# Kernel tuning notes

Measured on AMD Instinct MI355X. Metric: run time of the kernel, lower is better.

Reference implementation:

```python
import jax, jax.numpy as jnp
import numpy as np

H = 256          # hidden_dim
K = 5            # num_mixtures
Z = 32           # latent_dim
A = 3            # action dim
B, T = 128, 512
IN = Z + A       # LSTM input features
MDN = K * (1 + 2 * Z)  # 325


def setup_inputs() -> dict:
    key = jax.random.key(0)
    ks = jax.random.split(key, 8)
    s_in = 1.0 / np.sqrt(IN)
    s_h = 1.0 / np.sqrt(H)
    return {
        "z_t": jax.random.normal(ks[0], (B, T, Z), jnp.float32),
        "a_t": jax.random.normal(ks[1], (B, T, A), jnp.float32),
        # LSTM params: fused gate kernels, gate order [i, f, g, o]
        "Wx": jax.random.normal(ks[2], (IN, 4 * H), jnp.float32) * s_in,
        "Wh": jax.random.normal(ks[3], (H, 4 * H), jnp.float32) * s_h,
        "b": jnp.zeros((4 * H,), jnp.float32),
        # MDN head Dense(325)
        "Wd": jax.random.normal(ks[4], (H, MDN), jnp.float32) * s_h,
        "bd": jnp.zeros((MDN,), jnp.float32),
    }


def _mdnrnn(z_t, a_t, Wx, Wh, b, Wd, bd):
    x = jnp.concatenate([z_t, a_t], axis=-1)          # (B,T,IN)
    # hoist the input projection out of the recurrence (same math)
    xproj = jnp.einsum("bti,ig->btg", x, Wx)          # (B,T,4H)
    xproj_t = jnp.swapaxes(xproj, 0, 1)               # (T,B,4H)
    bsz = x.shape[0]
    c0 = jnp.zeros((bsz, H), x.dtype)
    h0 = jnp.zeros((bsz, H), x.dtype)

    def step(carry, xp):
        c, h = carry
        gates = xp + h @ Wh + b                        # (B,4H)
        i, f, g, o = jnp.split(gates, 4, axis=-1)
        i = jax.nn.sigmoid(i)
        f = jax.nn.sigmoid(f)
        g = jnp.tanh(g)
        o = jax.nn.sigmoid(o)
        c = f * c + i * g
        h = o * jnp.tanh(c)
        return (c, h), h

    final_carry, hs = jax.lax.scan(step, (c0, h0), xproj_t)
    outputs = jnp.swapaxes(hs, 0, 1)                  # (B,T,H)

    mdn = outputs @ Wd + bd                           # (B,T,325)
    log_pi, mu, log_sigma = jnp.split(mdn, [K, K + K * Z * 2 // 2 + K * Z - K], axis=-1)
    # splits: [K, (1+Z)*K] -> log_pi (K), mu (K*Z), log_sigma (K*Z)
    log_pi, mu, log_sigma = mdn[..., :K], mdn[..., K:K + K * Z], mdn[..., K + K * Z:]
    bt = outputs.shape[:2]
    mu = mu.reshape(bt[0], bt[1], K, Z)
    log_sigma = log_sigma.reshape(bt[0], bt[1], K, Z)
    log_pi = jax.nn.log_softmax(log_pi, axis=-1)
    sigma = jnp.exp(log_sigma) + 1e-06
    return log_pi, mu, sigma, final_carry


def reference(z_t, a_t, Wx, Wh, b, Wd, bd):
    return _mdnrnn(z_t, a_t, Wx, Wh, b, Wd, bd)
```

## Files before the change

kernel.cpp:

```cpp
#include <hip/hip_runtime.h>
#include <hip/hip_bf16.h>
#include <math.h>

#define T_LEN 512
#define B_SZ  128
#define H_DIM 256
#define G_DIM 1024
#define IN_D  35
#define MDN_D 325
#define K_MIX 5

#define NSLICE 4
#define BG     2
#define NGRP   64

static constexpr long OFF_MU    = 327680L;
static constexpr long OFF_SIGMA = 10813440L;
static constexpr long OFF_C     = 21299200L;
static constexpr long OFF_H     = 21331968L;

static constexpr size_t WS_OUT = 0;
static constexpr size_t WS_HG  = 33554432;

typedef unsigned uint2v  __attribute__((ext_vector_type(2)));
typedef float    float2v __attribute__((ext_vector_type(2)));
typedef float    float4v __attribute__((ext_vector_type(4)));

__device__ __forceinline__ float fast_sigmoid(float x) { return 1.0f / (1.0f + __expf(-x)); }
__device__ __forceinline__ float fast_tanh(float x) {
    return 1.0f - 2.0f / (__expf(2.0f * x) + 1.0f);
}

__device__ __forceinline__ void pk_fma_lo(float2v& acc, float2v w, float2v h) {
    asm("v_pk_fma_f32 %0, %1, %2, %0 op_sel:[0,0,0] op_sel_hi:[1,0,1]"
        : "+v"(acc) : "v"(w), "v"(h));
}
__device__ __forceinline__ void pk_fma_hi(float2v& acc, float2v w, float2v h) {
    asm("v_pk_fma_f32 %0, %1, %2, %0 op_sel:[0,1,0] op_sel_hi:[1,1,1]"
        : "+v"(acc) : "v"(w), "v"(h));
}

__global__ __launch_bounds__(512, 1) void lstm6_kernel(
    const float* __restrict__ z_t, const float* __restrict__ a_t,
    const float* __restrict__ Wx,  const float* __restrict__ Wh,
    const float* __restrict__ bias,
    float* __restrict__ h_glb,
    __hip_bfloat16* __restrict__ outs,
    float* __restrict__ out_c, float* __restrict__ out_h)
{
    const int bid = blockIdx.x;
    const int gr  = bid & 63;
    const int s   = bid >> 6;
    const int tid = threadIdx.x;
    const int cg  = tid >> 2;
    const int kq  = tid & 3;
    const int lc0 = cg * 2;
    const int gate = lc0 >> 6;
    const int j0   = lc0 & 63;
    const int gcol0 = gate * 256 + s * 64 + j0;

    __shared__ __align__(16) float h_lds[BG][4][68];
    __shared__ __align__(16) float x_lds[BG][44];
    __shared__ __align__(16) float g_red[BG][256];

    for (int i = tid; i < BG * 4 * 68; i += 512) ((float*)h_lds)[i] = 0.0f;
    if (tid < BG * 9) { int b = tid / 9, k = tid - 9 * b; x_lds[b][35 + k] = 0.0f; }

    float2v W2[64];
    #pragma unroll
    for (int i = 0; i < 64; ++i) {
        const size_t r = (size_t)(kq * 64 + i) * G_DIM;
        W2[i].x = Wh[r + gcol0];
        W2[i].y = Wh[r + gcol0 + 1];
    }
    float2v X2[10];
    #pragma unroll
    for (int i = 0; i < 10; ++i) {
        int xk = kq * 10 + i;
        bool ok = (xk < IN_D);
        X2[i].x = ok ? Wx[(size_t)xk * G_DIM + gcol0]     : 0.0f;
        X2[i].y = ok ? Wx[(size_t)xk * G_DIM + gcol0 + 1] : 0.0f;
    }
    #pragma unroll
    for (int i = 0; i < 64; ++i) asm volatile("" : "+v"(W2[i]));
    #pragma unroll
    for (int i = 0; i < 10; ++i) asm volatile("" : "+v"(X2[i]));

    const int cb = tid >> 6;
    const int cj = tid & 63;
    const float bc0 = bias[0 * 256 + s * 64 + cj];
    const float bc1 = bias[1 * 256 + s * 64 + cj];
    const float bc2 = bias[2 * 256 + s * 64 + cj];
    const float bc3 = bias[3 * 256 + s * 64 + cj];
    float c_reg = 0.0f;

    const int q  = tid - 128;
    const int pb = (q >= 96) ? 1 : 0;
    const int pp = q - 96 * pb;
    const int pk0 = pp * 2;
    const int pkk = pk0 + ((pk0 >= s * 64) ? 64 : 0);

    const int batch0 = gr * BG;
    float* hg = h_glb + (size_t)gr * (2 * BG * H_DIM);

    if (tid >= 384 && tid < 448) {
        int qq = tid - 384, b = qq >> 5, k = qq & 31;
        x_lds[b][k] = z_t[((size_t)(batch0 + b) * T_LEN + 0) * 32 + k];
    } else if (tid >= 448 && tid < 448 + BG * 3) {
        int qq = tid - 448, b = (qq >= 3), k = qq - 3 * b;
        x_lds[b][32 + k] = a_t[((size_t)(batch0 + b) * T_LEN + 0) * 3 + k];
    }
    __syncthreads();

    for (int t = 0; t < T_LEN; ++t) {
        if (t > 0 && tid >= 128 && tid < 320) {
            const unsigned want = (unsigned)((t - 1) & 3);
            const float* ap = hg + ((t - 1) & 1) * (BG * H_DIM) + pb * H_DIM + pkk;
            uint2v u;
            do {
                asm volatile("global_load_dwordx2 %0, %1, off sc0 sc1\n\t"
                             "s_waitcnt vmcnt(0)"
                             : "=v"(u) : "v"(ap) : "memory");
            } while ((u.x & 3u) != want || (u.y & 3u) != want);
            float* dst = &h_lds[pb][pkk >> 6][pkk & 63];
            dst[0] = __uint_as_float(u.x);
            dst[1] = __uint_as_float(u.y);
        }
        __syncthreads();

        float2v acc0 = {0.0f, 0.0f}, acc1 = {0.0f, 0.0f};
        {
            const float4v* hp0 = (const float4v*)h_lds[0][kq];
            const float4v* hp1 = (const float4v*)h_lds[1][kq];
            #pragma unroll
            for (int i4 = 0; i4 < 16; ++i4) {
                float4v hv0 = hp0[i4];
                float4v hv1 = hp1[i4];
                float2v h0lo = __builtin_shufflevector(hv0, hv0, 0, 1);
                float2v h0hi = __builtin_shufflevector(hv0, hv0, 2, 3);
                float2v h1lo = __builtin_shufflevector(hv1, hv1, 0, 1);
                float2v h1hi = __builtin_shufflevector(hv1, hv1, 2, 3);
                pk_fma_lo(acc0, W2[4*i4+0], h0lo); pk_fma_lo(acc1, W2[4*i4+0], h1lo);
                pk_fma_hi(acc0, W2[4*i4+1], h0lo); pk_fma_hi(acc1, W2[4*i4+1], h1lo);
                pk_fma_lo(acc0, W2[4*i4+2], h0hi); pk_fma_lo(acc1, W2[4*i4+2], h1hi);
                pk_fma_hi(acc0, W2[4*i4+3], h0hi); pk_fma_hi(acc1, W2[4*i4+3], h1hi);
            }
            #pragma unroll
            for (int i = 0; i < 5; ++i) {
                float2v xv0 = *(const float2v*)&x_lds[0][kq * 10 + 2 * i];
                float2v xv1 = *(const float2v*)&x_lds[1][kq * 10 + 2 * i];
                pk_fma_lo(acc0, X2[2*i],   xv0); pk_fma_lo(acc1, X2[2*i],   xv1);
                pk_fma_hi(acc0, X2[2*i+1], xv0); pk_fma_hi(acc1, X2[2*i+1], xv1);
            }
        }
        float a00 = acc0.x, a01 = acc0.y, a10 = acc1.x, a11 = acc1.y;
        a00 += __shfl_xor(a00, 1, 64); a00 += __shfl_xor(a00, 2, 64);
        a01 += __shfl_xor(a01, 1, 64); a01 += __shfl_xor(a01, 2, 64);
        a10 += __shfl_xor(a10, 1, 64); a10 += __shfl_xor(a10, 2, 64);
        a11 += __shfl_xor(a11, 1, 64); a11 += __shfl_xor(a11, 2, 64);
        if (kq == 0) {
            g_red[0][lc0] = a00; g_red[0][lc0 + 1] = a01;
            g_red[1][lc0] = a10; g_red[1][lc0 + 1] = a11;
        }
        __syncthreads();

        if (tid < 128) {
            float gi = g_red[cb][      cj] + bc0;
            float gf = g_red[cb][ 64 + cj] + bc1;
            float gg = g_red[cb][128 + cj] + bc2;
            float go = g_red[cb][192 + cj] + bc3;
            float iv = fast_sigmoid(gi), fv = fast_sigmoid(gf), ov = fast_sigmoid(go);
            float gv = fast_tanh(gg);
            c_reg = fmaf(fv, c_reg, iv * gv);
            float hv = ov * fast_tanh(c_reg);
            unsigned u = (__float_as_uint(hv) & ~3u) | (unsigned)(t & 3);
            float* dst = hg + (t & 1) * (BG * H_DIM) + cb * H_DIM + s * 64 + cj;
            asm volatile("global_store_dword %0, %1, off sc0 sc1"
                         :: "v"(dst), "v"(u) : "memory");
            h_lds[cb][s][cj] = __uint_as_float(u);
            outs[((size_t)(batch0 + cb) * T_LEN + t) * H_DIM + s * 64 + cj] =
                __float2bfloat16(hv);
            if (t == T_LEN - 1) {
                out_c[(batch0 + cb) * H_DIM + s * 64 + cj] = c_reg;
                out_h[(batch0 + cb) * H_DIM + s * 64 + cj] = hv;
            }
        }
        if (t + 1 < T_LEN) {
            if (tid >= 384 && tid < 448) {
                int qq = tid - 384, b = qq >> 5, k = qq & 31;
                x_lds[b][k] = z_t[((size_t)(batch0 + b) * T_LEN + (t + 1)) * 32 + k];
            } else if (tid >= 448 && tid < 448 + BG * 3) {
                int qq = tid - 448, b = (qq >= 3), k = qq - 3 * b;
                x_lds[b][32 + k] = a_t[((size_t)(batch0 + b) * T_LEN + (t + 1)) * 3 + k];
            }
        }
    }
}

__global__ __launch_bounds__(256, 1) void mdn_kernel(
    const unsigned short* __restrict__ outputs, const float* __restrict__ Wd,
    const float* __restrict__ bd, float* __restrict__ out)
{
    __shared__ __align__(16) float hT[H_DIM * 16];
    __shared__ float lp[16][K_MIX];

    const int tid = threadIdx.x;
    const long row0 = (long)blockIdx.x * 16;

    for (int idx = tid; idx < H_DIM * 16; idx += 256) {
        int r = idx >> 8;
        int k = idx & (H_DIM - 1);
        unsigned int u = outputs[(row0 + r) * H_DIM + k];
        hT[k * 16 + r] = __uint_as_float(u << 16);
    }
    __syncthreads();

    const int  cA = tid;
    const int  cB = tid + 256;
    const bool vB = (cB < MDN_D);
    const float bA = bd[cA];
    const float bB = vB ? bd[cB] : 0.0f;
    float accA[16], accB[16];
    #pragma unroll
    for (int r = 0; r < 16; ++r) { accA[r] = bA; accB[r] = bB; }

    for (int k = 0; k < H_DIM; ++k) {
        float wA = Wd[(size_t)k * MDN_D + cA];
        float wB = vB ? Wd[(size_t)k * MDN_D + cB] : 0.0f;
        const float4* hp = (const float4*)(hT + k * 16);
        float4 h0 = hp[0], h1 = hp[1], h2 = hp[2], h3 = hp[3];
        float hr[16] = { h0.x,h0.y,h0.z,h0.w, h1.x,h1.y,h1.z,h1.w,
                         h2.x,h2.y,h2.z,h2.w, h3.x,h3.y,h3.z,h3.w };
        #pragma unroll
        for (int r = 0; r < 16; ++r) {
            accA[r] = fmaf(hr[r], wA, accA[r]);
            accB[r] = fmaf(hr[r], wB, accB[r]);
        }
    }

    float* out_mu = out + OFF_MU;
    float* out_sg = out + OFF_SIGMA;
    #pragma unroll
    for (int r = 0; r < 16; ++r) {
        long row = row0 + r;
        float v = accA[r];
        if (cA < K_MIX)            lp[r][cA] = v;
        else if (cA < K_MIX + 160) out_mu[row * 160 + (cA - K_MIX)] = v;
        else                       out_sg[row * 160 + (cA - 165)]   = __expf(v) + 1e-6f;
        if (vB)                    out_sg[row * 160 + (cB - 165)]   = __expf(accB[r]) + 1e-6f;
    }
    __syncthreads();

    if (tid < 16) {
        int r = tid;
        long row = row0 + r;
        float v0 = lp[r][0], v1 = lp[r][1], v2 = lp[r][2], v3 = lp[r][3], v4 = lp[r][4];
        float m = fmaxf(fmaxf(fmaxf(v0, v1), fmaxf(v2, v3)), v4);
        float sum = __expf(v0-m) + __expf(v1-m) + __expf(v2-m) + __expf(v3-m) + __expf(v4-m);
        float ls = m + __logf(sum);
        out[row*5 + 0] = v0 - ls;
        out[row*5 + 1] = v1 - ls;
        out[row*5 + 2] = v2 - ls;
        out[row*5 + 3] = v3 - ls;
        out[row*5 + 4] = v4 - ls;
    }
}

extern "C" void kernel_launch(void* const* d_in, const int* in_sizes, int n_in,
                              void* d_out, int out_size, void* d_ws, size_t ws_size,
                              hipStream_t stream)
{
    const float* z_t = (const float*)d_in[0];
    const float* a_t = (const float*)d_in[1];
    const float* Wx  = (const float*)d_in[2];
    const float* Wh  = (const float*)d_in[3];
    const float* b   = (const float*)d_in[4];
    const float* Wd  = (const float*)d_in[5];
    const float* bd  = (const float*)d_in[6];
    float* out = (float*)d_out;

    char* ws = (char*)d_ws;
    __hip_bfloat16* outs = (__hip_bfloat16*)(ws + WS_OUT);
    float* h_glb         = (float*)(ws + WS_HG);

    lstm6_kernel<<<NGRP * NSLICE, 512, 0, stream>>>(z_t, a_t, Wx, Wh, b,
                                                    h_glb, outs,
                                                    out + OFF_C, out + OFF_H);
    mdn_kernel<<<(B_SZ * T_LEN) / 16, 256, 0, stream>>>((const unsigned short*)outs,
                                                        Wd, bd, out);
}
```

Measured before the change: 1.192 ms.

## Pipeline spin-wait loads, double-buffer x input, widen MDN tile with packed FMA

The LSTM spin-wait on neighbouring slices' h values now keeps two global loads in flight instead of issuing one and waiting for it, which should cut polling latency on the serial recurrence. The per-step x input buffer in LDS is double-buffered so the prefetch of step t+1 cannot race with reads of step t. The MDN head kernel now handles 32 rows per block, uses a padded transposed LDS tile (stride 34), and accumulates with float2 vector FMAs that may map to packed FP32 math. This raises occupancy hints and reuse of each Wd load. The trade-offs are more register pressure in the MDN kernel and extra memory traffic from the speculative polling loads.

```diff
diff --git a/kernel.cpp b/kernel.cpp
--- a/kernel.cpp
+++ b/kernel.cpp
@@ -40,7 +40,7 @@
         : "+v"(acc) : "v"(w), "v"(h));
 }
 
-__global__ __launch_bounds__(512, 1) void lstm6_kernel(
+__global__ __launch_bounds__(512, 1) void lstm9_kernel(
     const float* __restrict__ z_t, const float* __restrict__ a_t,
     const float* __restrict__ Wx,  const float* __restrict__ Wh,
     const float* __restrict__ bias,
@@ -60,11 +60,14 @@
     const int gcol0 = gate * 256 + s * 64 + j0;
 
     __shared__ __align__(16) float h_lds[BG][4][68];
-    __shared__ __align__(16) float x_lds[BG][44];
+    __shared__ __align__(16) float x_lds[2][BG][44];
     __shared__ __align__(16) float g_red[BG][256];
 
     for (int i = tid; i < BG * 4 * 68; i += 512) ((float*)h_lds)[i] = 0.0f;
-    if (tid < BG * 9) { int b = tid / 9, k = tid - 9 * b; x_lds[b][35 + k] = 0.0f; }
+    if (tid < 2 * BG * 9) {
+        int buf = tid / 18, r = tid % 18, b = r / 9, k = 35 + r % 9;
+        x_lds[buf][b][k] = 0.0f;
+    }
 
     float2v W2[64];
     #pragma unroll
@@ -105,10 +108,10 @@
 
     if (tid >= 384 && tid < 448) {
         int qq = tid - 384, b = qq >> 5, k = qq & 31;
-        x_lds[b][k] = z_t[((size_t)(batch0 + b) * T_LEN + 0) * 32 + k];
+        x_lds[0][b][k] = z_t[((size_t)(batch0 + b) * T_LEN + 0) * 32 + k];
     } else if (tid >= 448 && tid < 448 + BG * 3) {
         int qq = tid - 448, b = (qq >= 3), k = qq - 3 * b;
-        x_lds[b][32 + k] = a_t[((size_t)(batch0 + b) * T_LEN + 0) * 3 + k];
+        x_lds[0][b][32 + k] = a_t[((size_t)(batch0 + b) * T_LEN + 0) * 3 + k];
     }
     __syncthreads();
 
@@ -116,15 +119,23 @@
         if (t > 0 && tid >= 128 && tid < 320) {
             const unsigned want = (unsigned)((t - 1) & 3);
             const float* ap = hg + ((t - 1) & 1) * (BG * H_DIM) + pb * H_DIM + pkk;
-            uint2v u;
-            do {
-                asm volatile("global_load_dwordx2 %0, %1, off sc0 sc1\n\t"
-                             "s_waitcnt vmcnt(0)"
-                             : "=v"(u) : "v"(ap) : "memory");
-            } while ((u.x & 3u) != want || (u.y & 3u) != want);
+            uint2v u0, u1, got;
+            asm volatile("global_load_dwordx2 %0, %1, off sc0 sc1"
+                         : "=v"(u0) : "v"(ap) : "memory");
+            for (;;) {
+                asm volatile("global_load_dwordx2 %0, %1, off sc0 sc1"
+                             : "=v"(u1) : "v"(ap) : "memory");
+                asm volatile("s_waitcnt vmcnt(1)" : "+v"(u0) :: "memory");
+                if ((u0.x & 3u) == want && (u0.y & 3u) == want) { got = u0; break; }
+                asm volatile("global_load_dwordx2 %0, %1, off sc0 sc1"
+                             : "=v"(u0) : "v"(ap) : "memory");
+                asm volatile("s_waitcnt vmcnt(1)" : "+v"(u1) :: "memory");
+                if ((u1.x & 3u) == want && (u1.y & 3u) == want) { got = u1; break; }
+            }
+            asm volatile("s_waitcnt vmcnt(0)" ::: "memory");
             float* dst = &h_lds[pb][pkk >> 6][pkk & 63];
-            dst[0] = __uint_as_float(u.x);
-            dst[1] = __uint_as_float(u.y);
+            dst[0] = __uint_as_float(got.x);
+            dst[1] = __uint_as_float(got.y);
         }
         __syncthreads();
 
@@ -147,8 +158,8 @@
             }
             #pragma unroll
             for (int i = 0; i < 5; ++i) {
-                float2v xv0 = *(const float2v*)&x_lds[0][kq * 10 + 2 * i];
-                float2v xv1 = *(const float2v*)&x_lds[1][kq * 10 + 2 * i];
+                float2v xv0 = *(const float2v*)&x_lds[t & 1][0][kq * 10 + 2 * i];
+                float2v xv1 = *(const float2v*)&x_lds[t & 1][1][kq * 10 + 2 * i];
                 pk_fma_lo(acc0, X2[2*i],   xv0); pk_fma_lo(acc1, X2[2*i],   xv1);
                 pk_fma_hi(acc0, X2[2*i+1], xv0); pk_fma_hi(acc1, X2[2*i+1], xv1);
             }
@@ -188,30 +199,33 @@
         if (t + 1 < T_LEN) {
             if (tid >= 384 && tid < 448) {
                 int qq = tid - 384, b = qq >> 5, k = qq & 31;
-                x_lds[b][k] = z_t[((size_t)(batch0 + b) * T_LEN + (t + 1)) * 32 + k];
+                x_lds[(t + 1) & 1][b][k] =
+                    z_t[((size_t)(batch0 + b) * T_LEN + (t + 1)) * 32 + k];
             } else if (tid >= 448 && tid < 448 + BG * 3) {
                 int qq = tid - 448, b = (qq >= 3), k = qq - 3 * b;
-                x_lds[b][32 + k] = a_t[((size_t)(batch0 + b) * T_LEN + (t + 1)) * 3 + k];
-            }
-        }
-    }
-}
-
-__global__ __launch_bounds__(256, 1) void mdn_kernel(
+                x_lds[(t + 1) & 1][b][32 + k] =
+                    a_t[((size_t)(batch0 + b) * T_LEN + (t + 1)) * 3 + k];
+            }
+        }
+    }
+}
+
+#define MROWS 32
+__global__ __launch_bounds__(256, 4) void mdn2_kernel(
     const unsigned short* __restrict__ outputs, const float* __restrict__ Wd,
     const float* __restrict__ bd, float* __restrict__ out)
 {
-    __shared__ __align__(16) float hT[H_DIM * 16];
-    __shared__ float lp[16][K_MIX];
+    __shared__ __align__(16) float hT[H_DIM * 34];
+    __shared__ float lp[MROWS][K_MIX];
 
     const int tid = threadIdx.x;
-    const long row0 = (long)blockIdx.x * 16;
-
-    for (int idx = tid; idx < H_DIM * 16; idx += 256) {
+    const long row0 = (long)blockIdx.x * MROWS;
+
+    for (int idx = tid; idx < H_DIM * MROWS; idx += 256) {
         int r = idx >> 8;
         int k = idx & (H_DIM - 1);
-        unsigned int u = outputs[(row0 + r) * H_DIM + k];
-        hT[k * 16 + r] = __uint_as_float(u << 16);
+        unsigned u = outputs[(row0 + r) * H_DIM + k];
+        hT[k * 34 + r] = __uint_as_float(u << 16);
     }
     __syncthreads();
 
@@ -220,38 +234,47 @@
     const bool vB = (cB < MDN_D);
     const float bA = bd[cA];
     const float bB = vB ? bd[cB] : 0.0f;
-    float accA[16], accB[16];
-    #pragma unroll
-    for (int r = 0; r < 16; ++r) { accA[r] = bA; accB[r] = bB; }
+    float2v accA[16], accB[16];
+    #pragma unroll
+    for (int p = 0; p < 16; ++p) {
+        accA[p].x = bA; accA[p].y = bA;
+        accB[p].x = bB; accB[p].y = bB;
+    }
 
     for (int k = 0; k < H_DIM; ++k) {
         float wA = Wd[(size_t)k * MDN_D + cA];
         float wB = vB ? Wd[(size_t)k * MDN_D + cB] : 0.0f;
-        const float4* hp = (const float4*)(hT + k * 16);
-        float4 h0 = hp[0], h1 = hp[1], h2 = hp[2], h3 = hp[3];
-        float hr[16] = { h0.x,h0.y,h0.z,h0.w, h1.x,h1.y,h1.z,h1.w,
-                         h2.x,h2.y,h2.z,h2.w, h3.x,h3.y,h3.z,h3.w };
+        float2v wA2; wA2.x = wA; wA2.y = wA;
+        float2v wB2; wB2.x = wB; wB2.y = wB;
+        const float2v* hp = (const float2v*)(hT + k * 34);
         #pragma unroll
-        for (int r = 0; r < 16; ++r) {
-            accA[r] = fmaf(hr[r], wA, accA[r]);
-            accB[r] = fmaf(hr[r], wB, accB[r]);
+        for (int p = 0; p < 16; ++p) {
+            float2v h2 = hp[p];
+            accA[p] += h2 * wA2;
+            accB[p] += h2 * wB2;
         }
     }
 
     float* out_mu = out + OFF_MU;
     float* out_sg = out + OFF_SIGMA;
     #pragma unroll
-    for (int r = 0; r < 16; ++r) {
-        long row = row0 + r;
-        float v = accA[r];
-        if (cA < K_MIX)            lp[r][cA] = v;
-        else if (cA < K_MIX + 160) out_mu[row * 160 + (cA - K_MIX)] = v;
-        else                       out_sg[row * 160 + (cA - 165)]   = __expf(v) + 1e-6f;
-        if (vB)                    out_sg[row * 160 + (cB - 165)]   = __expf(accB[r]) + 1e-6f;
+    for (int p = 0; p < 16; ++p) {
+        #pragma unroll
+        for (int e = 0; e < 2; ++e) {
+            long row = row0 + 2 * p + e;
+            float v = e ? accA[p].y : accA[p].x;
+            if (cA < K_MIX)            lp[2*p+e][cA] = v;
+            else if (cA < K_MIX + 160) out_mu[row * 160 + (cA - K_MIX)] = v;
+            else                       out_sg[row * 160 + (cA - 165)]   = __expf(v) + 1e-6f;
+            if (vB) {
+                float vb = e ? accB[p].y : accB[p].x;
+                out_sg[row * 160 + (cB - 165)] = __expf(vb) + 1e-6f;
+            }
+        }
     }
     __syncthreads();
 
-    if (tid < 16) {
+    if (tid < MROWS) {
         int r = tid;
         long row = row0 + r;
         float v0 = lp[r][0], v1 = lp[r][1], v2 = lp[r][2], v3 = lp[r][3], v4 = lp[r][4];
@@ -283,9 +306,9 @@
     __hip_bfloat16* outs = (__hip_bfloat16*)(ws + WS_OUT);
     float* h_glb         = (float*)(ws + WS_HG);
 
-    lstm6_kernel<<<NGRP * NSLICE, 512, 0, stream>>>(z_t, a_t, Wx, Wh, b,
+    lstm9_kernel<<<NGRP * NSLICE, 512, 0, stream>>>(z_t, a_t, Wx, Wh, b,
                                                     h_glb, outs,
                                                     out + OFF_C, out + OFF_H);
-    mdn_kernel<<<(B_SZ * T_LEN) / 16, 256, 0, stream>>>((const unsigned short*)outs,
-                                                        Wd, bd, out);
-}
+    mdn2_kernel<<<(B_SZ * T_LEN) / MROWS, 256, 0, stream>>>((const unsigned short*)outs,
+                                                            Wd, bd, out);
+}
```

Result: slower. 1.234 ms (+3.5%).
